# Kernel tuning notes

Hardware: AMD Instinct MI355X
Metric: run time of the kernel (lower is better)

Reference implementation:

```python
import jax, jax.numpy as jnp
import numpy as np

B, S, D, H = 2, 2048, 2048, 16
HD = D // H            # 128
HALF = HD // 2         # 64
SOFTCAP = 50.0
ROPE_BASE = 10000.0


def setup_inputs() -> dict:
    key = jax.random.key(0)
    k1, k2, k3 = jax.random.split(key, 3)
    inputs = jax.random.normal(k1, (B, S, D), dtype=jnp.float32)
    # param init ~ nnx.initializers.normal() (stddev 0.01 default; scale to keep activations sane)
    w_in = jax.random.normal(k2, (D, H, 3 * HD), dtype=jnp.float32) * (1.0 / np.sqrt(D))
    w_out = jax.random.normal(k3, (H, HD, D), dtype=jnp.float32) * (1.0 / np.sqrt(D))
    # RoPE tables: [S, HALF]
    pos = jnp.arange(S, dtype=jnp.float32)[:, None]
    inv_freq = 1.0 / (ROPE_BASE ** (jnp.arange(HALF, dtype=jnp.float32) / HALF))
    ang = pos * inv_freq[None, :]
    rope_sin = jnp.sin(ang)
    rope_cos = jnp.cos(ang)
    # causal mask [1, 1, S, S]
    mask = jnp.tril(jnp.ones((S, S), dtype=bool))[None, None, :, :]
    return {"inputs": inputs, "w_in": w_in, "w_out": w_out,
            "rope_sin": rope_sin, "rope_cos": rope_cos, "mask": mask}


def apply_rope(x, sin, cos):
    # x: [B, S, H, HD]; sin/cos: [S, HALF] -> broadcast [1, S, 1, HALF]
    sin = sin[None, :, None, :]
    cos = cos[None, :, None, :]
    x1, x2 = x[..., :HALF], x[..., HALF:]
    return jnp.concatenate([x1 * cos - x2 * sin, x2 * cos + x1 * sin], axis=-1)


def reference(inputs, w_in, w_out, rope_sin, rope_cos, mask):
    dtype = inputs.dtype
    # fused QKV projection: [B, S, H, 3*HD]
    qkv = jnp.einsum('bsd,bhf->bshf'.replace('bhf', 'dhf'), inputs, w_in)
    q, k, v = jnp.split(qkv, 3, axis=-1)           # each [B, S, H, HD]
    q = apply_rope(q, rope_sin, rope_cos)
    k = apply_rope(k, rope_sin, rope_cos)
    q = q / jnp.sqrt(jnp.asarray(HD, dtype))
    scores = jnp.einsum('bqhd,bkhd->bhqk', q, k)   # [B, H, S, S]
    big_neg = jnp.finfo(dtype).min
    scores = jnp.where(mask, scores, big_neg)
    scores = jnp.tanh(scores / SOFTCAP) * SOFTCAP  # softcap
    attn = jax.nn.softmax(scores, axis=-1)
    x = jnp.einsum('bhqk,bkhd->bqhd', attn, v)     # [B, S, H, HD]
    out = jnp.einsum('bqhd,hdm->bqm', x, w_out)    # [B, S, D]
    return out
```

## Files before the change

kernel.cpp:

```cpp
#include <hip/hip_runtime.h>

#define B_ 2
#define S_ 2048
#define D_ 2048
#define H_ 16
#define HD_ 128
#define NT_ (S_ / 64)

typedef unsigned short u16;
typedef __bf16 bf16x8 __attribute__((ext_vector_type(8)));
typedef float f32x4 __attribute__((ext_vector_type(4)));

__device__ __forceinline__ float bf2f(u16 u) {
  unsigned int x = ((unsigned int)u) << 16;
  return __builtin_bit_cast(float, x);
}
__device__ __forceinline__ u16 f2bf(float f) {
  unsigned int u = __builtin_bit_cast(unsigned int, f);
  u += 0x7fffu + ((u >> 16) & 1u);
  return (u16)(u >> 16);
}
__device__ __forceinline__ void async16(const void* g, void* l) {
  __builtin_amdgcn_global_load_lds((const __attribute__((address_space(1))) void*)g,
                                   (__attribute__((address_space(3))) void*)l, 16, 0, 0);
}
__device__ __forceinline__ float vexp2(float x) {
  float r;
  asm("v_exp_f32 %0, %1" : "=v"(r) : "v"(x));
  return r;
}
__device__ __forceinline__ float vrcp(float x) {
  float r;
  asm("v_rcp_f32 %0, %1" : "=v"(r) : "v"(x));
  return r;
}

__global__ __launch_bounds__(256) void conv_f32_bf16(const float* __restrict__ in,
                                                     u16* __restrict__ outp, int n) {
  int idx = (blockIdx.x * 256 + threadIdx.x) * 4;
  int stride = gridDim.x * 256 * 4;
  for (; idx < n; idx += stride) {
    float4 v = *(const float4*)(in + idx);
    ushort4 ov = make_ushort4(f2bf(v.x), f2bf(v.y), f2bf(v.z), f2bf(v.w));
    *(ushort4*)(outp + idx) = ov;
  }
}

__global__ __launch_bounds__(256) void transpose_conv(const float* __restrict__ in,
                                                      u16* __restrict__ outp, int R, int C) {
  __shared__ float tile[32][33];
  int c0 = blockIdx.x * 32, r0 = blockIdx.y * 32;
  int tx = threadIdx.x & 31, ty = threadIdx.x >> 5;
#pragma unroll
  for (int yy = 0; yy < 32; yy += 8)
    tile[ty + yy][tx] = in[(size_t)(r0 + ty + yy) * C + c0 + tx];
  __syncthreads();
#pragma unroll
  for (int yy = 0; yy < 32; yy += 8)
    outp[(size_t)(c0 + ty + yy) * R + r0 + tx] = f2bf(tile[tx][ty + yy]);
}

__global__ __launch_bounds__(256) void transpose_v(const u16* __restrict__ in,
                                                   u16* __restrict__ outp) {
  __shared__ u16 tile[32][33];
  int bhh = blockIdx.z;
  const u16* ip = in + (size_t)bhh * S_ * HD_;
  u16* op = outp + (size_t)bhh * HD_ * S_;
  int hd0 = blockIdx.x * 32, s0 = blockIdx.y * 32;
  int tx = threadIdx.x & 31, ty = threadIdx.x >> 5;
#pragma unroll
  for (int yy = 0; yy < 32; yy += 8)
    tile[ty + yy][tx] = ip[(size_t)(s0 + ty + yy) * HD_ + hd0 + tx];
  __syncthreads();
#pragma unroll
  for (int yy = 0; yy < 32; yy += 8)
    op[(size_t)(hd0 + ty + yy) * S_ + s0 + tx] = tile[tx][ty + yy];
}

__global__ __launch_bounds__(256) void rope_kernel(u16* __restrict__ Q, u16* __restrict__ Kk,
                                                   const float* __restrict__ rsin,
                                                   const float* __restrict__ rcos) {
  int t = blockIdx.x * 256 + threadIdx.x;
  u16* base = blockIdx.y ? Kk : Q;
  float scale = blockIdx.y ? 1.0f : 0.08838834764831845f;
  int row = t >> 3, seg = t & 7;
  int s = row & (S_ - 1);
  int i0 = seg * 8;
  u16* p = base + (size_t)row * HD_;
  alignas(16) u16 x1[8], x2[8], o1[8], o2[8];
  *(uint4*)x1 = *(const uint4*)(p + i0);
  *(uint4*)x2 = *(const uint4*)(p + 64 + i0);
  alignas(16) float sn[8], cs[8];
  *(float4*)sn = *(const float4*)(rsin + s * 64 + i0);
  *(float4*)(sn + 4) = *(const float4*)(rsin + s * 64 + i0 + 4);
  *(float4*)cs = *(const float4*)(rcos + s * 64 + i0);
  *(float4*)(cs + 4) = *(const float4*)(rcos + s * 64 + i0 + 4);
#pragma unroll
  for (int j = 0; j < 8; ++j) {
    float a = bf2f(x1[j]), bb = bf2f(x2[j]);
    o1[j] = f2bf((a * cs[j] - bb * sn[j]) * scale);
    o2[j] = f2bf((bb * cs[j] + a * sn[j]) * scale);
  }
  *(uint4*)(p + i0) = *(uint4*)o1;
  *(uint4*)(p + 64 + i0) = *(uint4*)o2;
}

template <int EPI>
__global__ __launch_bounds__(256) void gemm_bt(const u16* __restrict__ A, const u16* __restrict__ Bt,
                                               float* __restrict__ C, int M, int N, int K,
                                               u16* __restrict__ Qo, u16* __restrict__ Ko,
                                               u16* __restrict__ Vo) {
  __shared__ alignas(16) u16 lsA[128 * 32];
  __shared__ alignas(16) u16 lsB[128 * 32];
  const int tid = threadIdx.x;
  const int lane = tid & 63, wid = tid >> 6;
  const int g = lane >> 4, lr = lane & 15;
  const int wr = wid >> 1, wc = wid & 1;
  const int m0 = blockIdx.y * 128, n0 = blockIdx.x * 128;
  f32x4 acc[4][4] = {};
  const int nk = K >> 5;
  for (int kt = 0; kt < nk; ++kt) {
    const int k0 = kt << 5;
    __syncthreads();
#pragma unroll
    for (int p = 0; p < 2; ++p) {
      const int c = p * 256 + tid;
      const int row = c >> 2;
      const int wb = (c & 3) << 4;
      async16((const char*)(A + (size_t)(m0 + row) * K + k0) + wb, (char*)lsA + c * 16);
      async16((const char*)(Bt + (size_t)(n0 + row) * K + k0) + wb, (char*)lsB + c * 16);
    }
    __syncthreads();
    bf16x8 af[4], bfr[4];
#pragma unroll
    for (int i = 0; i < 4; ++i)
      af[i] = *(const bf16x8*)((const char*)lsA + (wr * 64 + i * 16 + lr) * 64 + g * 16);
#pragma unroll
    for (int j = 0; j < 4; ++j)
      bfr[j] = *(const bf16x8*)((const char*)lsB + (wc * 64 + j * 16 + lr) * 64 + g * 16);
#pragma unroll
    for (int i = 0; i < 4; ++i)
#pragma unroll
      for (int j = 0; j < 4; ++j)
        acc[i][j] = __builtin_amdgcn_mfma_f32_16x16x32_bf16(af[i], bfr[j], acc[i][j], 0, 0, 0);
  }
  if (EPI == 0) {
#pragma unroll
    for (int i = 0; i < 4; ++i)
#pragma unroll
      for (int j = 0; j < 4; ++j)
#pragma unroll
        for (int r = 0; r < 4; ++r) {
          int m = m0 + wr * 64 + i * 16 + 4 * g + r;
          int n = n0 + wc * 64 + j * 16 + lr;
          C[(size_t)m * N + n] = acc[i][j][r];
        }
  } else {
    const int t = blockIdx.x;
    const int part = t % 3, h = t / 3;
    u16* dst = (part == 0) ? Qo : (part == 1 ? Ko : Vo);
#pragma unroll
    for (int i = 0; i < 4; ++i)
#pragma unroll
      for (int j = 0; j < 4; ++j)
#pragma unroll
        for (int r = 0; r < 4; ++r) {
          int m = m0 + wr * 64 + i * 16 + 4 * g + r;
          int hd = wc * 64 + j * 16 + lr;
          int b = m >> 11, s = m & (S_ - 1);
          dst[((size_t)(b * H_ + h) * S_ + s) * HD_ + hd] = f2bf(acc[i][j][r]);
        }
  }
}

__global__ __launch_bounds__(256) void attn_fwd(const u16* __restrict__ Q, const u16* __restrict__ K,
                                                const u16* __restrict__ VT, u16* __restrict__ X) {
  const int bx = blockIdx.x;
  const int bh = blockIdx.y;
  const int tid = threadIdx.x;
  const int lane = tid & 63, wid = tid >> 6;
  const int g = lane >> 4, lr = lane & 15;

  __shared__ alignas(16) u16 lsK[2][64 * 128];
  __shared__ alignas(16) u16 lsV[2][128 * 64];
  __shared__ alignas(16) u16 lsP[4][16 * 72];

  const u16* Qp = Q + (size_t)bh * S_ * HD_;
  const u16* Kp = K + (size_t)bh * S_ * HD_;
  const u16* Vp = VT + (size_t)bh * HD_ * S_;
  u16* myP = lsP[wid];
  const int b = bh >> 4, h = bh & 15;

  const float c1 = -0.057707802f;
  const float c2 = -144.26950409f;

#pragma unroll 1
  for (int pass = 0; pass < 2; ++pass) {
    const int qt = pass ? bx : (NT_ - 1 - bx);
    const int qrow = qt * 64 + wid * 16 + lr;
    const int qbase = qt * 64 + wid * 16 + 4 * g;

    bf16x8 qf[4];
#pragma unroll
    for (int kc = 0; kc < 4; ++kc)
      qf[kc] = *(const bf16x8*)(Qp + (size_t)qrow * HD_ + kc * 32 + g * 8);

    f32x4 o[8] = {};
    float psum[4] = {0.f, 0.f, 0.f, 0.f};

#pragma unroll
    for (int p = 0; p < 4; ++p) {
      int c = p * 256 + tid;
      int rowk = c >> 4;
      int wsk = ((c & 15) << 4) ^ ((rowk & 7) << 4);
      async16((const char*)Kp + (((size_t)rowk) << 8) + wsk, (char*)lsK[0] + c * 16);
      int rowv = c >> 3;
      int wsv = ((c & 7) << 4) ^ ((rowv & 7) << 4);
      async16((const char*)Vp + (size_t)rowv * (S_ * 2) + wsv, (char*)lsV[0] + c * 16);
    }
    __syncthreads();

    int cur = 0;
    for (int kt = 0; kt <= qt; ++kt) {
      if (kt < qt) {
        const int nxt = kt + 1;
#pragma unroll
        for (int p = 0; p < 4; ++p) {
          int c = p * 256 + tid;
          int rowk = c >> 4;
          int wsk = ((c & 15) << 4) ^ ((rowk & 7) << 4);
          async16((const char*)Kp + (((size_t)(nxt * 64 + rowk)) << 8) + wsk,
                  (char*)lsK[cur ^ 1] + c * 16);
          int rowv = c >> 3;
          int wsv = ((c & 7) << 4) ^ ((rowv & 7) << 4);
          async16((const char*)Vp + (size_t)rowv * (S_ * 2) + nxt * 128 + wsv,
                  (char*)lsV[cur ^ 1] + c * 16);
        }
      }
      f32x4 sc[4];
#pragma unroll
      for (int jn = 0; jn < 4; ++jn) {
        f32x4 a = {0.f, 0.f, 0.f, 0.f};
        const int row = jn * 16 + lr;
        const int sw = (row & 7) << 4;
#pragma unroll
        for (int kc = 0; kc < 4; ++kc) {
          int w = (kc * 64 + g * 16) ^ sw;
          bf16x8 kf = *(const bf16x8*)((const char*)lsK[cur] + row * 256 + w);
          a = __builtin_amdgcn_mfma_f32_16x16x32_bf16(qf[kc], kf, a, 0, 0, 0);
        }
        sc[jn] = a;
      }
#pragma unroll
      for (int jn = 0; jn < 4; ++jn) {
        int key = kt * 64 + jn * 16 + lr;
#pragma unroll
        for (int r = 0; r < 4; ++r) {
          float z = vexp2(c1 * sc[jn][r]);
          float p = vexp2(c2 * z * vrcp(1.f + z));
          if (key > qbase + r) p = 0.f;
          psum[r] += p;
          myP[(4 * g + r) * 72 + jn * 16 + lr] = f2bf(p);
        }
      }
#pragma unroll
      for (int kc = 0; kc < 2; ++kc) {
        bf16x8 pa = *(const bf16x8*)(myP + lr * 72 + kc * 32 + g * 8);
#pragma unroll
        for (int jh = 0; jh < 8; ++jh) {
          int row = jh * 16 + lr;
          int w = (kc * 64 + g * 16) ^ ((row & 7) << 4);
          bf16x8 vf = *(const bf16x8*)((const char*)lsV[cur] + row * 128 + w);
          o[jh] = __builtin_amdgcn_mfma_f32_16x16x32_bf16(pa, vf, o[jh], 0, 0, 0);
        }
      }
      __syncthreads();
      cur ^= 1;
    }
    float lsum[4];
#pragma unroll
    for (int r = 0; r < 4; ++r) {
      float s = psum[r];
#pragma unroll
      for (int msk = 1; msk < 16; msk <<= 1) s += __shfl_xor(s, msk, 64);
      lsum[r] = s;
    }
#pragma unroll
    for (int r = 0; r < 4; ++r) {
      float inv = 1.f / lsum[r];
      int s = qbase + r;
      u16* xp = X + ((size_t)(b * S_ + s)) * D_ + h * HD_;
#pragma unroll
      for (int jh = 0; jh < 8; ++jh) xp[jh * 16 + lr] = f2bf(o[jh][r] * inv);
    }
  }
}

extern "C" void kernel_launch(void* const* d_in, const int* in_sizes, int n_in,
                              void* d_out, int out_size, void* d_ws, size_t ws_size,
                              hipStream_t stream) {
  const float* inputs = (const float*)d_in[0];
  const float* w_in = (const float*)d_in[1];
  const float* w_out = (const float*)d_in[2];
  const float* rsin = (const float*)d_in[3];
  const float* rcos = (const float*)d_in[4];
  float* out = (float*)d_out;

  char* ws = (char*)d_ws;
  u16* bfA = (u16*)(ws);
  u16* w_inT = (u16*)(ws + 16777216);
  u16* Qraw = (u16*)(ws + 41943040);
  u16* Kraw = (u16*)(ws + 58720256);
  u16* Vraw = (u16*)(ws + 75497472);
  u16* VT = (u16*)(ws + 92274688);
  u16* Xbuf = (u16*)(ws);
  u16* w_outT = (u16*)(ws + 16777216);

  conv_f32_bf16<<<2048, 256, 0, stream>>>(inputs, bfA, B_ * S_ * D_);
  transpose_conv<<<dim3(6144 / 32, 2048 / 32), 256, 0, stream>>>(w_in, w_inT, 2048, 6144);
  gemm_bt<1><<<dim3(48, 32), 256, 0, stream>>>(bfA, w_inT, nullptr, 4096, 6144, 2048,
                                               Qraw, Kraw, Vraw);
  transpose_conv<<<dim3(2048 / 32, 2048 / 32), 256, 0, stream>>>(w_out, w_outT, 2048, 2048);
  rope_kernel<<<dim3(2048, 2), 256, 0, stream>>>(Qraw, Kraw, rsin, rcos);
  transpose_v<<<dim3(4, 64, 32), 256, 0, stream>>>(Vraw, VT);
  attn_fwd<<<dim3(NT_ / 2, 32), 256, 0, stream>>>(Qraw, Kraw, VT, Xbuf);
  gemm_bt<0><<<dim3(16, 32), 256, 0, stream>>>(Xbuf, w_outT, out, 4096, 2048, 2048,
                                               nullptr, nullptr, nullptr);
}
```

Measured before the change: 319.5 us.

## Rewrite GEMMs with pipelined 128x256 tiles, fuse RoPE and V transpose into epilogue

Replaces the simple 128x128 GEMM with a 512-thread 128x256 tile kernel. It uses a triple-buffered async LDS pipeline with XOR swizzling, split MFMA phases with priority hints, and a block-index swizzle. The QKV projection epilogue now applies RoPE and the Q scaling directly and writes V transposed, so the separate rope and transpose_v kernels go away. Weight columns are permuted during the transpose so each lane holds matching RoPE pairs, and attention output stores are vectorized to match the permuted w_out layout. This cuts kernel launches and intermediate memory traffic, at the cost of complex index permutations that must stay consistent across kernels.

```diff
diff --git a/kernel.cpp b/kernel.cpp
--- a/kernel.cpp
+++ b/kernel.cpp
@@ -10,6 +10,7 @@
 typedef unsigned short u16;
 typedef __bf16 bf16x8 __attribute__((ext_vector_type(8)));
 typedef float f32x4 __attribute__((ext_vector_type(4)));
+typedef u16 u16x8 __attribute__((ext_vector_type(8)));
 
 __device__ __forceinline__ float bf2f(u16 u) {
   unsigned int x = ((unsigned int)u) << 16;
@@ -46,130 +47,232 @@
   }
 }
 
-__global__ __launch_bounds__(256) void transpose_conv(const float* __restrict__ in,
-                                                      u16* __restrict__ outp, int R, int C) {
+__global__ __launch_bounds__(256) void transpose_win(const float* __restrict__ in,
+                                                     u16* __restrict__ outp) {
   __shared__ float tile[32][33];
-  int c0 = blockIdx.x * 32, r0 = blockIdx.y * 32;
+  int n0 = blockIdx.x * 32, k0 = blockIdx.y * 32;
   int tx = threadIdx.x & 31, ty = threadIdx.x >> 5;
+  int n = n0 + tx;
+  int cc = n >> 7, p = n & 127;
+  int q = (p >> 4) & 3;
+  int d = ((p >> 6) << 5) + ((q >> 1) << 4) + ((q & 1) << 6) + (p & 15);
+  int f = (cc / 3) * 384 + (cc % 3) * 128 + d;
 #pragma unroll
   for (int yy = 0; yy < 32; yy += 8)
-    tile[ty + yy][tx] = in[(size_t)(r0 + ty + yy) * C + c0 + tx];
+    tile[ty + yy][tx] = in[(size_t)(k0 + ty + yy) * 6144 + f];
   __syncthreads();
 #pragma unroll
   for (int yy = 0; yy < 32; yy += 8)
-    outp[(size_t)(c0 + ty + yy) * R + r0 + tx] = f2bf(tile[tx][ty + yy]);
-}
-
-__global__ __launch_bounds__(256) void transpose_v(const u16* __restrict__ in,
-                                                   u16* __restrict__ outp) {
-  __shared__ u16 tile[32][33];
-  int bhh = blockIdx.z;
-  const u16* ip = in + (size_t)bhh * S_ * HD_;
-  u16* op = outp + (size_t)bhh * HD_ * S_;
-  int hd0 = blockIdx.x * 32, s0 = blockIdx.y * 32;
+    outp[(size_t)(n0 + ty + yy) * 2048 + k0 + tx] = f2bf(tile[tx][ty + yy]);
+}
+
+__global__ __launch_bounds__(256) void transpose_wout(const float* __restrict__ in,
+                                                      u16* __restrict__ outp) {
+  __shared__ float tile[32][33];
+  int k0 = blockIdx.x * 32, n0 = blockIdx.y * 32;
   int tx = threadIdx.x & 31, ty = threadIdx.x >> 5;
 #pragma unroll
+  for (int yy = 0; yy < 32; yy += 8) {
+    int kk = k0 + ty + yy;
+    int hh = kk >> 7, j = kk & 127;
+    int hd = (j & 7) * 16 + (j >> 3);
+    tile[ty + yy][tx] = in[(size_t)(hh * 128 + hd) * 2048 + n0 + tx];
+  }
+  __syncthreads();
+#pragma unroll
   for (int yy = 0; yy < 32; yy += 8)
-    tile[ty + yy][tx] = ip[(size_t)(s0 + ty + yy) * HD_ + hd0 + tx];
-  __syncthreads();
-#pragma unroll
-  for (int yy = 0; yy < 32; yy += 8)
-    op[(size_t)(hd0 + ty + yy) * S_ + s0 + tx] = tile[tx][ty + yy];
-}
-
-__global__ __launch_bounds__(256) void rope_kernel(u16* __restrict__ Q, u16* __restrict__ Kk,
-                                                   const float* __restrict__ rsin,
-                                                   const float* __restrict__ rcos) {
-  int t = blockIdx.x * 256 + threadIdx.x;
-  u16* base = blockIdx.y ? Kk : Q;
-  float scale = blockIdx.y ? 1.0f : 0.08838834764831845f;
-  int row = t >> 3, seg = t & 7;
-  int s = row & (S_ - 1);
-  int i0 = seg * 8;
-  u16* p = base + (size_t)row * HD_;
-  alignas(16) u16 x1[8], x2[8], o1[8], o2[8];
-  *(uint4*)x1 = *(const uint4*)(p + i0);
-  *(uint4*)x2 = *(const uint4*)(p + 64 + i0);
-  alignas(16) float sn[8], cs[8];
-  *(float4*)sn = *(const float4*)(rsin + s * 64 + i0);
-  *(float4*)(sn + 4) = *(const float4*)(rsin + s * 64 + i0 + 4);
-  *(float4*)cs = *(const float4*)(rcos + s * 64 + i0);
-  *(float4*)(cs + 4) = *(const float4*)(rcos + s * 64 + i0 + 4);
-#pragma unroll
-  for (int j = 0; j < 8; ++j) {
-    float a = bf2f(x1[j]), bb = bf2f(x2[j]);
-    o1[j] = f2bf((a * cs[j] - bb * sn[j]) * scale);
-    o2[j] = f2bf((bb * cs[j] + a * sn[j]) * scale);
-  }
-  *(uint4*)(p + i0) = *(uint4*)o1;
-  *(uint4*)(p + 64 + i0) = *(uint4*)o2;
-}
+    outp[(size_t)(n0 + ty + yy) * 2048 + k0 + tx] = f2bf(tile[tx][ty + yy]);
+}
+
+#define BAR __builtin_amdgcn_s_barrier()
+#define LGKM0                                          \
+  {                                                    \
+    asm volatile("s_waitcnt lgkmcnt(0)" ::: "memory"); \
+    __builtin_amdgcn_sched_barrier(0);                 \
+  }
+#define VM6 asm volatile("s_waitcnt vmcnt(6)" ::: "memory")
+#define VM0 asm volatile("s_waitcnt vmcnt(0)" ::: "memory")
+#define P1 __builtin_amdgcn_s_setprio(1)
+#define P0 __builtin_amdgcn_s_setprio(0)
 
 template <int EPI>
-__global__ __launch_bounds__(256) void gemm_bt(const u16* __restrict__ A, const u16* __restrict__ Bt,
-                                               float* __restrict__ C, int M, int N, int K,
-                                               u16* __restrict__ Qo, u16* __restrict__ Ko,
-                                               u16* __restrict__ Vo) {
-  __shared__ alignas(16) u16 lsA[128 * 32];
-  __shared__ alignas(16) u16 lsB[128 * 32];
+__global__ __launch_bounds__(512, 1) void gemm128(
+    const u16* __restrict__ A, const u16* __restrict__ Bt, float* __restrict__ C, int K, int N,
+    int ntn, u16* __restrict__ Qo, u16* __restrict__ Ko, u16* __restrict__ Vo,
+    const float* __restrict__ rsin, const float* __restrict__ rcos) {
+  __shared__ alignas(16) u16 lsA[3][128 * 64];
+  __shared__ alignas(16) u16 lsB[3][256 * 64];
   const int tid = threadIdx.x;
   const int lane = tid & 63, wid = tid >> 6;
   const int g = lane >> 4, lr = lane & 15;
-  const int wr = wid >> 1, wc = wid & 1;
-  const int m0 = blockIdx.y * 128, n0 = blockIdx.x * 128;
+  const int wm = wid >> 2, wn = wid & 3;
+
+  const int nwg = ntn << 5;
+  const int bid = blockIdx.x;
+  const int swz = (bid & 7) * (nwg >> 3) + (bid >> 3);
+  const int m_idx = swz & 31, n_idx = swz >> 5;
+  const size_t m0 = (size_t)m_idx * 128, n0 = (size_t)n_idx * 256;
+
+  const int rowq = tid >> 3, slq = tid & 7;
+  const int kofs = (slq ^ (rowq & 7)) << 3;
+  const u16* pA0 = A + (m0 + rowq) * K + kofs;
+  const u16* pA1 = A + (m0 + 64 + rowq) * K + kofs;
+  const u16* pB0 = Bt + (n0 + rowq) * K + kofs;
+  const u16* pB1 = Bt + (n0 + 64 + rowq) * K + kofs;
+  const u16* pB2 = Bt + (n0 + 128 + rowq) * K + kofs;
+  const u16* pB3 = Bt + (n0 + 192 + rowq) * K + kofs;
+
+#define STG_A(t, buf)                                               \
+  {                                                                 \
+    async16(pA0 + (size_t)(t)*64, (char*)lsA[buf] + tid * 16);      \
+    async16(pA1 + (size_t)(t)*64, (char*)lsA[buf] + 8192 + tid * 16); \
+  }
+#define STG_B(t, buf)                                                  \
+  {                                                                    \
+    async16(pB0 + (size_t)(t)*64, (char*)lsB[buf] + tid * 16);         \
+    async16(pB1 + (size_t)(t)*64, (char*)lsB[buf] + 8192 + tid * 16);  \
+    async16(pB2 + (size_t)(t)*64, (char*)lsB[buf] + 16384 + tid * 16); \
+    async16(pB3 + (size_t)(t)*64, (char*)lsB[buf] + 24576 + tid * 16); \
+  }
+
+  const int sw0 = ((g) ^ (lr & 7)) << 4;
+  const int sw1 = ((4 + g) ^ (lr & 7)) << 4;
+
+#define LDA(tb)                                                              \
+  {                                                                          \
+    _Pragma("unroll") for (int i2 = 0; i2 < 4; ++i2) {                       \
+      const char* _p = (const char*)lsA[tb] + (wm * 64 + i2 * 16 + lr) * 128; \
+      aF[i2][0] = *(const bf16x8*)(_p + sw0);                                \
+      aF[i2][1] = *(const bf16x8*)(_p + sw1);                                \
+    }                                                                        \
+  }
+#define LDB(tb, dst, nh)                                                                \
+  {                                                                                     \
+    _Pragma("unroll") for (int j2 = 0; j2 < 2; ++j2) {                                  \
+      const char* _p = (const char*)lsB[tb] + (wn * 64 + (nh)*32 + j2 * 16 + lr) * 128; \
+      dst[j2][0] = *(const bf16x8*)(_p + sw0);                                          \
+      dst[j2][1] = *(const bf16x8*)(_p + sw1);                                          \
+    }                                                                                   \
+  }
+#define MM(nh, BB)                                                                           \
+  {                                                                                          \
+    _Pragma("unroll") for (int i2 = 0; i2 < 4; ++i2) _Pragma("unroll") for (int j2 = 0;     \
+                                                                            j2 < 2; ++j2) { \
+      acc[i2][(nh)*2 + j2] = __builtin_amdgcn_mfma_f32_16x16x32_bf16(                        \
+          aF[i2][0], BB[j2][0], acc[i2][(nh)*2 + j2], 0, 0, 0);                              \
+      acc[i2][(nh)*2 + j2] = __builtin_amdgcn_mfma_f32_16x16x32_bf16(                        \
+          aF[i2][1], BB[j2][1], acc[i2][(nh)*2 + j2], 0, 0, 0);                              \
+    }                                                                                        \
+  }
+
   f32x4 acc[4][4] = {};
-  const int nk = K >> 5;
+  const int nk = K >> 6;
+
+  STG_A(0, 0);
+  STG_B(0, 0);
+  STG_A(1, 1);
+  STG_B(1, 1);
+  VM6;
+  BAR;
+
+  bf16x8 aF[4][2], b01[2][2], b23[2][2];
+#pragma unroll 1
   for (int kt = 0; kt < nk; ++kt) {
-    const int k0 = kt << 5;
-    __syncthreads();
-#pragma unroll
-    for (int p = 0; p < 2; ++p) {
-      const int c = p * 256 + tid;
-      const int row = c >> 2;
-      const int wb = (c & 3) << 4;
-      async16((const char*)(A + (size_t)(m0 + row) * K + k0) + wb, (char*)lsA + c * 16);
-      async16((const char*)(Bt + (size_t)(n0 + row) * K + k0) + wb, (char*)lsB + c * 16);
-    }
-    __syncthreads();
-    bf16x8 af[4], bfr[4];
+    const int tb = kt % 3;
+    const int sb = (kt + 2) % 3;
+    const bool stg = (kt + 2) < nk;
+    LDA(tb);
+    LDB(tb, b01, 0);
+    if (stg) STG_A(kt + 2, sb);
+    BAR;
+    LGKM0;
+    P1;
+    MM(0, b01);
+    P0;
+    BAR;
+    LDB(tb, b23, 1);
+    if (stg) STG_B(kt + 2, sb);
+    BAR;
+    LGKM0;
+    P1;
+    MM(1, b23);
+    P0;
+    if (kt < nk - 2) {
+      VM6;
+    } else {
+      VM0;
+    }
+    BAR;
+  }
+#undef STG_A
+#undef STG_B
+#undef LDA
+#undef LDB
+#undef MM
+
+  if (EPI == 0) {
 #pragma unroll
     for (int i = 0; i < 4; ++i)
-      af[i] = *(const bf16x8*)((const char*)lsA + (wr * 64 + i * 16 + lr) * 64 + g * 16);
-#pragma unroll
-    for (int j = 0; j < 4; ++j)
-      bfr[j] = *(const bf16x8*)((const char*)lsB + (wc * 64 + j * 16 + lr) * 64 + g * 16);
-#pragma unroll
-    for (int i = 0; i < 4; ++i)
 #pragma unroll
       for (int j = 0; j < 4; ++j)
-        acc[i][j] = __builtin_amdgcn_mfma_f32_16x16x32_bf16(af[i], bfr[j], acc[i][j], 0, 0, 0);
-  }
-  if (EPI == 0) {
-#pragma unroll
-    for (int i = 0; i < 4; ++i)
-#pragma unroll
-      for (int j = 0; j < 4; ++j)
 #pragma unroll
         for (int r = 0; r < 4; ++r) {
-          int m = m0 + wr * 64 + i * 16 + 4 * g + r;
-          int n = n0 + wc * 64 + j * 16 + lr;
-          C[(size_t)m * N + n] = acc[i][j][r];
+          size_t m = m0 + wm * 64 + i * 16 + 4 * g + r;
+          size_t n = n0 + wn * 64 + j * 16 + lr;
+          C[m * N + n] = acc[i][j][r];
         }
   } else {
-    const int t = blockIdx.x;
-    const int part = t % 3, h = t / 3;
-    u16* dst = (part == 0) ? Qo : (part == 1 ? Ko : Vo);
-#pragma unroll
-    for (int i = 0; i < 4; ++i)
-#pragma unroll
-      for (int j = 0; j < 4; ++j)
+    const int c = (int)(n0 >> 7) + (wn >> 1);
+    const int h = c / 3, part = c % 3;
+    const int wn1 = wn & 1;
+    if (part == 2) {
+#pragma unroll
+      for (int i = 0; i < 4; ++i) {
+        int m = (int)m0 + wm * 64 + i * 16 + 4 * g;
+        int b = m >> 11, s = m & (S_ - 1);
+#pragma unroll
+        for (int j = 0; j < 4; ++j) {
+          int hd = wn1 * 32 + ((j >> 1) << 4) + ((j & 1) << 6) + lr;
+          ushort4 pk;
+          pk.x = f2bf(acc[i][j][0]);
+          pk.y = f2bf(acc[i][j][1]);
+          pk.z = f2bf(acc[i][j][2]);
+          pk.w = f2bf(acc[i][j][3]);
+          *(ushort4*)(Vo + ((size_t)(b * H_ + h) * HD_ + hd) * S_ + s) = pk;
+        }
+      }
+    } else {
+      u16* dstp = (part == 0) ? Qo : Ko;
+      const float scl = (part == 0) ? 0.08838834764831845f : 1.0f;
+#pragma unroll
+      for (int i = 0; i < 4; ++i) {
+        int mbase = (int)m0 + wm * 64 + i * 16 + 4 * g;
 #pragma unroll
         for (int r = 0; r < 4; ++r) {
-          int m = m0 + wr * 64 + i * 16 + 4 * g + r;
-          int hd = wc * 64 + j * 16 + lr;
+          int m = mbase + r;
           int b = m >> 11, s = m & (S_ - 1);
-          dst[((size_t)(b * H_ + h) * S_ + s) * HD_ + hd] = f2bf(acc[i][j][r]);
-        }
+          const float* srow = rsin + s * 64;
+          const float* crow = rcos + s * 64;
+          u16* op = dstp + ((size_t)(b * H_ + h) * S_ + s) * HD_ + ((wn1 * 16 + lr) << 2);
+          ushort4 pk;
+          {
+            int d = wn1 * 32 + lr;
+            float cv = crow[d] * scl, sv = srow[d] * scl;
+            float x1 = acc[i][0][r], x2 = acc[i][1][r];
+            pk.x = f2bf(x1 * cv - x2 * sv);
+            pk.y = f2bf(x2 * cv + x1 * sv);
+          }
+          {
+            int d = wn1 * 32 + 16 + lr;
+            float cv = crow[d] * scl, sv = srow[d] * scl;
+            float x1 = acc[i][2][r], x2 = acc[i][3][r];
+            pk.z = f2bf(x1 * cv - x2 * sv);
+            pk.w = f2bf(x2 * cv + x1 * sv);
+          }
+          *(ushort4*)op = pk;
+        }
+      }
+    }
   }
 }
 
@@ -289,9 +392,10 @@
     for (int r = 0; r < 4; ++r) {
       float inv = 1.f / lsum[r];
       int s = qbase + r;
-      u16* xp = X + ((size_t)(b * S_ + s)) * D_ + h * HD_;
-#pragma unroll
-      for (int jh = 0; jh < 8; ++jh) xp[jh * 16 + lr] = f2bf(o[jh][r] * inv);
+      u16x8 pk;
+#pragma unroll
+      for (int jh = 0; jh < 8; ++jh) pk[jh] = f2bf(o[jh][r] * inv);
+      *(u16x8*)(X + ((size_t)(b * S_ + s)) * D_ + h * HD_ + lr * 8) = pk;
     }
   }
 }
@@ -311,19 +415,16 @@
   u16* w_inT = (u16*)(ws + 16777216);
   u16* Qraw = (u16*)(ws + 41943040);
   u16* Kraw = (u16*)(ws + 58720256);
-  u16* Vraw = (u16*)(ws + 75497472);
-  u16* VT = (u16*)(ws + 92274688);
+  u16* VT = (u16*)(ws + 75497472);
   u16* Xbuf = (u16*)(ws);
   u16* w_outT = (u16*)(ws + 16777216);
 
   conv_f32_bf16<<<2048, 256, 0, stream>>>(inputs, bfA, B_ * S_ * D_);
-  transpose_conv<<<dim3(6144 / 32, 2048 / 32), 256, 0, stream>>>(w_in, w_inT, 2048, 6144);
-  gemm_bt<1><<<dim3(48, 32), 256, 0, stream>>>(bfA, w_inT, nullptr, 4096, 6144, 2048,
-                                               Qraw, Kraw, Vraw);
-  transpose_conv<<<dim3(2048 / 32, 2048 / 32), 256, 0, stream>>>(w_out, w_outT, 2048, 2048);
-  rope_kernel<<<dim3(2048, 2), 256, 0, stream>>>(Qraw, Kraw, rsin, rcos);
-  transpose_v<<<dim3(4, 64, 32), 256, 0, stream>>>(Vraw, VT);
+  transpose_win<<<dim3(192, 64), 256, 0, stream>>>(w_in, w_inT);
+  gemm128<1><<<768, 512, 0, stream>>>(bfA, w_inT, nullptr, 2048, 6144, 24, Qraw, Kraw, VT,
+                                      rsin, rcos);
+  transpose_wout<<<dim3(64, 64), 256, 0, stream>>>(w_out, w_outT);
   attn_fwd<<<dim3(NT_ / 2, 32), 256, 0, stream>>>(Qraw, Kraw, VT, Xbuf);
-  gemm_bt<0><<<dim3(16, 32), 256, 0, stream>>>(Xbuf, w_outT, out, 4096, 2048, 2048,
-                                               nullptr, nullptr, nullptr);
-}
+  gemm128<0><<<256, 512, 0, stream>>>(Xbuf, w_outT, out, 2048, 2048, 8,
+                                      nullptr, nullptr, nullptr, nullptr, nullptr);
+}
```

New measurement: 278.3 us. 12.9% less time.
